# Kernel tuning notes

Hardware: AMD Instinct MI355X
Metric: run time of the kernel (lower is better)

The kernel has to match this reference:

```python
import jax, jax.numpy as jnp
import numpy as np

D_MODEL = 1024
N_HEADS = 16
HEAD_DIM = D_MODEL // N_HEADS
NEG_INF = -1e10


def setup_inputs() -> dict:
    key = jax.random.key(0)
    ks = jax.random.split(key, 6)
    B, S = 2, 2048
    x = jax.random.normal(ks[0], (B, S, D_MODEL), dtype=jnp.float32)
    mask = jnp.ones((B, S), dtype=jnp.int32)
    scale_w = 1.0 / np.sqrt(D_MODEL)
    Wq = jax.random.normal(ks[1], (D_MODEL, D_MODEL), dtype=jnp.float32) * scale_w
    Wk = jax.random.normal(ks[2], (D_MODEL, D_MODEL), dtype=jnp.float32) * scale_w
    Wv = jax.random.normal(ks[3], (D_MODEL, D_MODEL), dtype=jnp.float32) * scale_w
    Wo = jax.random.normal(ks[4], (D_MODEL, D_MODEL), dtype=jnp.float32) * scale_w
    bq = jnp.zeros((D_MODEL,), jnp.float32)
    bk = jnp.zeros((D_MODEL,), jnp.float32)
    bv = jnp.zeros((D_MODEL,), jnp.float32)
    bo = jnp.zeros((D_MODEL,), jnp.float32)
    return {"x": x, "mask": mask, "Wq": Wq, "bq": bq, "Wk": Wk, "bk": bk,
            "Wv": Wv, "bv": bv, "Wo": Wo, "bo": bo}


def reference(x, mask, Wq, bq, Wk, bk, Wv, bv, Wo, bo):
    B, S, _ = x.shape
    # Linear projections (torch Linear: y = x @ W.T + b)
    Q = x @ Wq.T + bq
    K = x @ Wk.T + bk
    V = x @ Wv.T + bv
    # [B, H, S, Dh]
    Q = Q.reshape(B, S, N_HEADS, HEAD_DIM).transpose(0, 2, 1, 3)
    K = K.reshape(B, S, N_HEADS, HEAD_DIM).transpose(0, 2, 1, 3)
    V = V.reshape(B, S, N_HEADS, HEAD_DIM).transpose(0, 2, 1, 3)
    scale = jnp.sqrt(jnp.float32(HEAD_DIM))
    energy = jnp.einsum('bhqd,bhkd->bhqk', Q, K) / scale  # [B,H,S,S]
    # mask: [B,S] -> broadcast over heads and query dim (keys masked)
    m = mask[:, None, None, :]  # [B,1,1,S]
    energy = jnp.where(m == 0, jnp.float32(NEG_INF), energy)
    attention = jax.nn.softmax(energy, axis=-1)
    # dropout in eval mode = identity
    out = jnp.einsum('bhqk,bhkd->bhqd', attention, V)  # [B,H,S,Dh]
    out = out.transpose(0, 2, 1, 3).reshape(B, S, D_MODEL)
    return out @ Wo.T + bo
```

## Files before the change

### kernel.cpp

```cpp
#include <hip/hip_runtime.h>
#include <hip/hip_bf16.h>

typedef __hip_bfloat16 bf16;
typedef __attribute__((ext_vector_type(8))) short s8v;
typedef __attribute__((ext_vector_type(4))) float f4v;

#define D_MODEL 1024
#define S_LEN   2048
#define BATCH   2
#define NH      16
#define HD      64
#define M_TOTAL 4096

__device__ __forceinline__ void gll16(const bf16* g, bf16* l) {
    __builtin_amdgcn_global_load_lds(
        (const __attribute__((address_space(1))) void*)g,
        (__attribute__((address_space(3))) void*)l, 16, 0, 0);
}

__global__ __launch_bounds__(256) void cvt_bf16x8(const float* __restrict__ s,
                                                  bf16* __restrict__ d, int n) {
    int i = (blockIdx.x * 256 + threadIdx.x) * 8;
    if (i < n) {
        float4 a = *(const float4*)(s + i);
        float4 b = *(const float4*)(s + i + 4);
        union { bf16 h[8]; uint4 u; } p;
        p.h[0] = __float2bfloat16(a.x); p.h[1] = __float2bfloat16(a.y);
        p.h[2] = __float2bfloat16(a.z); p.h[3] = __float2bfloat16(a.w);
        p.h[4] = __float2bfloat16(b.x); p.h[5] = __float2bfloat16(b.y);
        p.h[6] = __float2bfloat16(b.z); p.h[7] = __float2bfloat16(b.w);
        *(uint4*)(d + i) = p.u;
    }
}

struct WPtrs { const float* s0; const float* s1; const float* s2; const float* s3;
               bf16* d0; bf16* d1; bf16* d2; bf16* d3; };

__global__ __launch_bounds__(256) void cvt_w(WPtrs p) {
    const float* s; bf16* d;
    switch (blockIdx.y) {
        case 0:  s = p.s0; d = p.d0; break;
        case 1:  s = p.s1; d = p.d1; break;
        case 2:  s = p.s2; d = p.d2; break;
        default: s = p.s3; d = p.d3; break;
    }
    int i = (blockIdx.x * 256 + threadIdx.x) * 8;
    float4 a = *(const float4*)(s + i);
    float4 b = *(const float4*)(s + i + 4);
    union { bf16 h[8]; uint4 u; } q;
    q.h[0] = __float2bfloat16(a.x); q.h[1] = __float2bfloat16(a.y);
    q.h[2] = __float2bfloat16(a.z); q.h[3] = __float2bfloat16(a.w);
    q.h[4] = __float2bfloat16(b.x); q.h[5] = __float2bfloat16(b.y);
    q.h[6] = __float2bfloat16(b.z); q.h[7] = __float2bfloat16(b.w);
    *(uint4*)(d + i) = q.u;
}

template<int TM, int TN>
__device__ __forceinline__ void gemm_main(const bf16* __restrict__ A,
                                          const bf16* __restrict__ W,
                                          bf16* As, bf16* Bs,
                                          int bm, int bn,
                                          f4v (&acc)[TM/32][TN/32])
{
    constexpr int FM = TM / 32, FN = TN / 32;
    constexpr int CALLS_A = TM / 16, CALLS = (TM + TN) / 16, PW = CALLS / 4;
    const int t = threadIdx.x, wv = t >> 6, lane = t & 63;
    const int quad = lane >> 4, l15 = lane & 15;
    const int wm = (wv >> 1) * (TM / 2), wn = (wv & 1) * (TN / 2);
    const int lr = lane >> 2, lc = (lane & 3) * 8;

    const bf16* aptr[FM];
    const bf16* bptr[FN];
    #pragma unroll
    for (int i = 0; i < FM; ++i) aptr[i] = As + (wm + i * 16 + l15) * 32 + quad * 8;
    #pragma unroll
    for (int j = 0; j < FN; ++j) bptr[j] = Bs + (wn + j * 16 + l15) * 32 + quad * 8;

    for (int k0 = 0; k0 < D_MODEL; k0 += 32) {
        __syncthreads();
        #pragma unroll
        for (int c = 0; c < PW; ++c) {
            const int cc = wv * PW + c;
            if (cc < CALLS_A) {
                gll16(A + (size_t)(bm + cc * 16 + lr) * D_MODEL + k0 + lc,
                      As + cc * 16 * 32);
            } else {
                const int r2 = cc - CALLS_A;
                gll16(W + (size_t)(bn + r2 * 16 + lr) * D_MODEL + k0 + lc,
                      Bs + r2 * 16 * 32);
            }
        }
        __syncthreads();

        s8v af[FM], bfv[FN];
        #pragma unroll
        for (int i = 0; i < FM; ++i) af[i] = *(const s8v*)aptr[i];
        #pragma unroll
        for (int j = 0; j < FN; ++j) bfv[j] = *(const s8v*)bptr[j];
        #pragma unroll
        for (int i = 0; i < FM; ++i)
            #pragma unroll
            for (int j = 0; j < FN; ++j)
                acc[i][j] = __builtin_amdgcn_mfma_f32_16x16x32_bf16(af[i], bfv[j], acc[i][j], 0, 0, 0);
    }
}

__global__ __launch_bounds__(256) void gemm_qkv(
    const bf16* __restrict__ x,
    const bf16* __restrict__ Wq, const bf16* __restrict__ Wk, const bf16* __restrict__ Wv,
    const float* __restrict__ bq, const float* __restrict__ bk, const float* __restrict__ bv,
    bf16* __restrict__ Qb, bf16* __restrict__ Kb, bf16* __restrict__ Vtb)
{
    __shared__ __align__(16) bf16 As[128 * 32];
    __shared__ __align__(16) bf16 Bs[128 * 32];
    const int z = blockIdx.z;
    const bf16*  W    = (z == 0) ? Wq : (z == 1) ? Wk : Wv;
    const float* bias = (z == 0) ? bq : (z == 1) ? bk : bv;
    bf16*        out  = (z == 0) ? Qb : (z == 1) ? Kb : Vtb;
    const int bm = blockIdx.y * 128, bn = blockIdx.x * 128;

    f4v acc[4][4] = {};
    gemm_main<128, 128>(x, W, As, Bs, bm, bn, acc);

    const int t = threadIdx.x, wv = t >> 6, lane = t & 63;
    const int quad = lane >> 4, l15 = lane & 15;
    const int wm = (wv >> 1) * 64, wn = (wv & 1) * 64;
    #pragma unroll
    for (int j = 0; j < 4; ++j) {
        const int col = bn + wn + j * 16 + l15;
        const float bv_ = bias[col];
        const int h = col >> 6, d = col & 63;
        #pragma unroll
        for (int i = 0; i < 4; ++i) {
            #pragma unroll
            for (int r = 0; r < 4; ++r) {
                const int row = bm + wm + i * 16 + quad * 4 + r;
                const int b = row >> 11, s = row & 2047;
                const float v = acc[i][j][r] + bv_;
                size_t idx;
                if (z == 2) idx = (((size_t)(b * NH + h)) * HD + d) * S_LEN + s;
                else        idx = (((size_t)(b * NH + h)) * S_LEN + s) * HD + d;
                out[idx] = __float2bfloat16(v);
            }
        }
    }
}

__global__ __launch_bounds__(256) void gemm_out(
    const bf16* __restrict__ Ob, const bf16* __restrict__ Wo,
    const float* __restrict__ bo, float* __restrict__ out)
{
    __shared__ __align__(16) bf16 As[64 * 32];
    __shared__ __align__(16) bf16 Bs[128 * 32];
    const int bm = blockIdx.y * 64, bn = blockIdx.x * 128;

    f4v acc[2][4] = {};
    gemm_main<64, 128>(Ob, Wo, As, Bs, bm, bn, acc);

    const int t = threadIdx.x, wv = t >> 6, lane = t & 63;
    const int quad = lane >> 4, l15 = lane & 15;
    const int wm = (wv >> 1) * 32, wn = (wv & 1) * 64;
    #pragma unroll
    for (int j = 0; j < 4; ++j) {
        const int col = bn + wn + j * 16 + l15;
        const float bv_ = bo[col];
        #pragma unroll
        for (int i = 0; i < 2; ++i)
            #pragma unroll
            for (int r = 0; r < 4; ++r) {
                const int row = bm + wm + i * 16 + quad * 4 + r;
                out[(size_t)row * D_MODEL + col] = acc[i][j][r] + bv_;
            }
    }
}

__global__ __launch_bounds__(256) void attn_mfma(
    const bf16* __restrict__ Q, const bf16* __restrict__ K,
    const bf16* __restrict__ Vt, const int* __restrict__ mask,
    bf16* __restrict__ O)
{
    __shared__ __align__(16) bf16 Ks[64][72];
    __shared__ __align__(16) bf16 Vts[64][72];
    __shared__ __align__(16) bf16 Ps[4][16][72];
    __shared__ __align__(16) int  msk[64];

    const int t = threadIdx.x, wv = t >> 6, lane = t & 63;
    const int quad = lane >> 4, l15 = lane & 15;
    const int qt = blockIdx.x & 31, h = (blockIdx.x >> 5) & 15, b = blockIdx.x >> 9;
    const int q0 = qt * 64;
    const size_t qkbase = ((size_t)(b * NH + h)) * S_LEN * HD;
    const size_t vtbase = ((size_t)(b * NH + h)) * HD * S_LEN;

    const bf16* qrow = Q + qkbase + (size_t)(q0 + wv * 16 + l15) * HD;
    const s8v qf0 = *(const s8v*)(qrow + quad * 8);
    const s8v qf1 = *(const s8v*)(qrow + 32 + quad * 8);

    const int srow = t >> 2, scoff = (t & 3) * 16;

    float mprev = -1e30f, lsum = 0.f;
    f4v oacc[4] = {};

    for (int kt = 0; kt < S_LEN / 64; ++kt) {
        const int k0 = kt * 64;
        __syncthreads();
        {
            const uint4* kp = (const uint4*)(K  + qkbase + (size_t)(k0 + srow) * HD + scoff);
            const uint4* vp = (const uint4*)(Vt + vtbase + (size_t)srow * S_LEN + k0 + scoff);
            uint4 ka = kp[0], kb2 = kp[1];
            uint4 va = vp[0], vb2 = vp[1];
            *(uint4*)&Ks[srow][scoff]      = ka;
            *(uint4*)&Ks[srow][scoff + 8]  = kb2;
            *(uint4*)&Vts[srow][scoff]     = va;
            *(uint4*)&Vts[srow][scoff + 8] = vb2;
            if (t < 64) msk[t] = mask[b * S_LEN + k0 + t];
        }
        __syncthreads();

        f4v st[4];
        #pragma unroll
        for (int c = 0; c < 4; ++c) {
            s8v kf0 = *(const s8v*)&Ks[c * 16 + l15][quad * 8];
            s8v kf1 = *(const s8v*)&Ks[c * 16 + l15][32 + quad * 8];
            f4v z = {0.f, 0.f, 0.f, 0.f};
            z = __builtin_amdgcn_mfma_f32_16x16x32_bf16(kf0, qf0, z, 0, 0, 0);
            z = __builtin_amdgcn_mfma_f32_16x16x32_bf16(kf1, qf1, z, 0, 0, 0);
            st[c] = z;
        }

        float mt = -1e30f;
        #pragma unroll
        for (int c = 0; c < 4; ++c) {
            const int4 mk = *(const int4*)&msk[c * 16 + quad * 4];
            float v0 = st[c][0] * 0.125f; if (mk.x == 0) v0 = -1e10f;
            float v1 = st[c][1] * 0.125f; if (mk.y == 0) v1 = -1e10f;
            float v2 = st[c][2] * 0.125f; if (mk.z == 0) v2 = -1e10f;
            float v3 = st[c][3] * 0.125f; if (mk.w == 0) v3 = -1e10f;
            st[c][0] = v0; st[c][1] = v1; st[c][2] = v2; st[c][3] = v3;
            mt = fmaxf(mt, fmaxf(fmaxf(v0, v1), fmaxf(v2, v3)));
        }
        mt = fmaxf(mt, __shfl_xor(mt, 16, 64));
        mt = fmaxf(mt, __shfl_xor(mt, 32, 64));

        const float mn = fmaxf(mprev, mt);
        const float alpha = __expf(mprev - mn);
        mprev = mn;

        float ps = 0.f;
        #pragma unroll
        for (int c = 0; c < 4; ++c) {
            #pragma unroll
            for (int r = 0; r < 4; ++r) {
                const float p = __expf(st[c][r] - mn);
                st[c][r] = p;
                ps += p;
            }
        }
        ps += __shfl_xor(ps, 16, 64);
        ps += __shfl_xor(ps, 32, 64);
        lsum = lsum * alpha + ps;

        #pragma unroll
        for (int c = 0; c < 4; ++c) {
            union { bf16 h[4]; short4 s4; } pk;
            pk.h[0] = __float2bfloat16(st[c][0]);
            pk.h[1] = __float2bfloat16(st[c][1]);
            pk.h[2] = __float2bfloat16(st[c][2]);
            pk.h[3] = __float2bfloat16(st[c][3]);
            *(short4*)&Ps[wv][l15][c * 16 + quad * 4] = pk.s4;
        }

        float av[4];
        #pragma unroll
        for (int r = 0; r < 4; ++r) av[r] = __shfl(alpha, quad * 4 + r, 64);
        #pragma unroll
        for (int dt = 0; dt < 4; ++dt)
            #pragma unroll
            for (int r = 0; r < 4; ++r) oacc[dt][r] *= av[r];

        s8v pf0 = *(const s8v*)&Ps[wv][l15][quad * 8];
        s8v pf1 = *(const s8v*)&Ps[wv][l15][32 + quad * 8];
        #pragma unroll
        for (int dt = 0; dt < 4; ++dt) {
            s8v vf0 = *(const s8v*)&Vts[dt * 16 + l15][quad * 8];
            s8v vf1 = *(const s8v*)&Vts[dt * 16 + l15][32 + quad * 8];
            oacc[dt] = __builtin_amdgcn_mfma_f32_16x16x32_bf16(pf0, vf0, oacc[dt], 0, 0, 0);
            oacc[dt] = __builtin_amdgcn_mfma_f32_16x16x32_bf16(pf1, vf1, oacc[dt], 0, 0, 0);
        }
    }

    float linv[4];
    #pragma unroll
    for (int r = 0; r < 4; ++r) linv[r] = 1.f / __shfl(lsum, quad * 4 + r, 64);
    #pragma unroll
    for (int dt = 0; dt < 4; ++dt) {
        #pragma unroll
        for (int r = 0; r < 4; ++r) {
            const int s = q0 + wv * 16 + quad * 4 + r;
            const int col = h * 64 + dt * 16 + l15;
            O[((size_t)b * S_LEN + s) * D_MODEL + col] = __float2bfloat16(oacc[dt][r] * linv[r]);
        }
    }
}

extern "C" void kernel_launch(void* const* d_in, const int* in_sizes, int n_in,
                              void* d_out, int out_size, void* d_ws, size_t ws_size,
                              hipStream_t stream) {
    const float* x    = (const float*)d_in[0];
    const int*   mask = (const int*)  d_in[1];
    const float* Wq   = (const float*)d_in[2];
    const float* bq   = (const float*)d_in[3];
    const float* Wk   = (const float*)d_in[4];
    const float* bk   = (const float*)d_in[5];
    const float* Wv   = (const float*)d_in[6];
    const float* bv   = (const float*)d_in[7];
    const float* Wo   = (const float*)d_in[8];
    const float* bo   = (const float*)d_in[9];
    float* out = (float*)d_out;

    char* w = (char*)d_ws;
    bf16* xb  = (bf16*)w; w += (size_t)M_TOTAL * D_MODEL * 2;
    bf16* Wqb = (bf16*)w; w += (size_t)D_MODEL * D_MODEL * 2;
    bf16* Wkb = (bf16*)w; w += (size_t)D_MODEL * D_MODEL * 2;
    bf16* Wvb = (bf16*)w; w += (size_t)D_MODEL * D_MODEL * 2;
    bf16* Wob = (bf16*)w; w += (size_t)D_MODEL * D_MODEL * 2;
    bf16* Qb  = (bf16*)w; w += (size_t)M_TOTAL * D_MODEL * 2;
    bf16* Kb  = (bf16*)w; w += (size_t)M_TOTAL * D_MODEL * 2;
    bf16* Vtb = (bf16*)w; w += (size_t)M_TOTAL * D_MODEL * 2;
    bf16* Ob  = (bf16*)w; w += (size_t)M_TOTAL * D_MODEL * 2;

    const int nx = M_TOTAL * D_MODEL;
    cvt_bf16x8<<<nx / 2048, 256, 0, stream>>>(x, xb, nx);
    WPtrs wp = { Wq, Wk, Wv, Wo, Wqb, Wkb, Wvb, Wob };
    cvt_w<<<dim3(D_MODEL * D_MODEL / 2048, 4), 256, 0, stream>>>(wp);

    gemm_qkv<<<dim3(8, 32, 3), 256, 0, stream>>>(xb, Wqb, Wkb, Wvb, bq, bk, bv, Qb, Kb, Vtb);

    attn_mfma<<<BATCH * NH * (S_LEN / 64), 256, 0, stream>>>(Qb, Kb, Vtb, mask, Ob);

    gemm_out<<<dim3(8, 64), 256, 0, stream>>>(Ob, Wob, bo, out);
}
```

Measured before the change: 240.7 us.

## Use direct-to-LDS loads in attention, swap MFMA operands, fold softmax scale into Q

The attention kernel now stages K and V^T tiles with global_load_lds in a 32-wide packed layout instead of loading through registers into padded shared arrays. The PV MFMA operands are swapped so each lane holds a whole query row, which removes the alpha and lsum shuffles and lets output stores be packed short4 writes. The QKV GEMM swaps operands for Q and K so its epilogue can write packed, vectorised bf16 values, and it folds the 1/sqrt(d) scale into Q. The unpadded LDS layout may add bank conflicts on the fragment reads.

```diff
diff --git a/kernel.cpp b/kernel.cpp
--- a/kernel.cpp
+++ b/kernel.cpp
@@ -12,11 +12,9 @@
 #define HD      64
 #define M_TOTAL 4096
 
-__device__ __forceinline__ void gll16(const bf16* g, bf16* l) {
-    __builtin_amdgcn_global_load_lds(
-        (const __attribute__((address_space(1))) void*)g,
-        (__attribute__((address_space(3))) void*)l, 16, 0, 0);
-}
+#define GLL(gp, lp) __builtin_amdgcn_global_load_lds(                           \
+    (const __attribute__((address_space(1))) void*)(gp),                        \
+    (__attribute__((address_space(3))) void*)(lp), 16, 0, 0)
 
 __global__ __launch_bounds__(256) void cvt_bf16x8(const float* __restrict__ s,
                                                   bf16* __restrict__ d, int n) {
@@ -55,8 +53,8 @@
     *(uint4*)(d + i) = q.u;
 }
 
-template<int TM, int TN>
-__device__ __forceinline__ void gemm_main(const bf16* __restrict__ A,
+template<int TM, int TN, bool SWAP>
+__device__ __forceinline__ void gemm_loop(const bf16* __restrict__ A,
                                           const bf16* __restrict__ W,
                                           bf16* As, bf16* Bs,
                                           int bm, int bn,
@@ -76,18 +74,19 @@
     #pragma unroll
     for (int j = 0; j < FN; ++j) bptr[j] = Bs + (wn + j * 16 + l15) * 32 + quad * 8;
 
+    const bf16* ag = A + (size_t)(bm + lr) * D_MODEL + lc;
+    const bf16* wg = W + (size_t)(bn + lr) * D_MODEL + lc;
+
     for (int k0 = 0; k0 < D_MODEL; k0 += 32) {
         __syncthreads();
         #pragma unroll
         for (int c = 0; c < PW; ++c) {
             const int cc = wv * PW + c;
             if (cc < CALLS_A) {
-                gll16(A + (size_t)(bm + cc * 16 + lr) * D_MODEL + k0 + lc,
-                      As + cc * 16 * 32);
+                GLL(ag + (size_t)cc * 16 * D_MODEL + k0, As + cc * 512);
             } else {
                 const int r2 = cc - CALLS_A;
-                gll16(W + (size_t)(bn + r2 * 16 + lr) * D_MODEL + k0 + lc,
-                      Bs + r2 * 16 * 32);
+                GLL(wg + (size_t)r2 * 16 * D_MODEL + k0, Bs + r2 * 512);
             }
         }
         __syncthreads();
@@ -100,8 +99,12 @@
         #pragma unroll
         for (int i = 0; i < FM; ++i)
             #pragma unroll
-            for (int j = 0; j < FN; ++j)
-                acc[i][j] = __builtin_amdgcn_mfma_f32_16x16x32_bf16(af[i], bfv[j], acc[i][j], 0, 0, 0);
+            for (int j = 0; j < FN; ++j) {
+                if (SWAP)
+                    acc[i][j] = __builtin_amdgcn_mfma_f32_16x16x32_bf16(bfv[j], af[i], acc[i][j], 0, 0, 0);
+                else
+                    acc[i][j] = __builtin_amdgcn_mfma_f32_16x16x32_bf16(af[i], bfv[j], acc[i][j], 0, 0, 0);
+            }
     }
 }
 
@@ -116,31 +119,49 @@
     const int z = blockIdx.z;
     const bf16*  W    = (z == 0) ? Wq : (z == 1) ? Wk : Wv;
     const float* bias = (z == 0) ? bq : (z == 1) ? bk : bv;
-    bf16*        out  = (z == 0) ? Qb : (z == 1) ? Kb : Vtb;
     const int bm = blockIdx.y * 128, bn = blockIdx.x * 128;
-
-    f4v acc[4][4] = {};
-    gemm_main<128, 128>(x, W, As, Bs, bm, bn, acc);
 
     const int t = threadIdx.x, wv = t >> 6, lane = t & 63;
     const int quad = lane >> 4, l15 = lane & 15;
     const int wm = (wv >> 1) * 64, wn = (wv & 1) * 64;
-    #pragma unroll
-    for (int j = 0; j < 4; ++j) {
-        const int col = bn + wn + j * 16 + l15;
-        const float bv_ = bias[col];
-        const int h = col >> 6, d = col & 63;
+
+    f4v acc[4][4] = {};
+    if (z == 2) {
+        gemm_loop<128, 128, false>(x, W, As, Bs, bm, bn, acc);
+        #pragma unroll
+        for (int j = 0; j < 4; ++j) {
+            const int n = bn + wn + j * 16 + l15;
+            const int h = n >> 6, d = n & 63;
+            const float bv_ = bias[n];
+            #pragma unroll
+            for (int i = 0; i < 4; ++i) {
+                const int m0 = bm + wm + i * 16 + quad * 4;
+                const int b = m0 >> 11, s0 = m0 & 2047;
+                union { bf16 hh[4]; short4 s4; } pk;
+                #pragma unroll
+                for (int r = 0; r < 4; ++r) pk.hh[r] = __float2bfloat16(acc[i][j][r] + bv_);
+                *(short4*)&Vtb[(((size_t)(b * NH + h)) * HD + d) * S_LEN + s0] = pk.s4;
+            }
+        }
+    } else {
+        gemm_loop<128, 128, true>(x, W, As, Bs, bm, bn, acc);
+        bf16* out = (z == 0) ? Qb : Kb;
+        const float scale = (z == 0) ? 0.125f : 1.0f;
         #pragma unroll
         for (int i = 0; i < 4; ++i) {
-            #pragma unroll
-            for (int r = 0; r < 4; ++r) {
-                const int row = bm + wm + i * 16 + quad * 4 + r;
-                const int b = row >> 11, s = row & 2047;
-                const float v = acc[i][j][r] + bv_;
-                size_t idx;
-                if (z == 2) idx = (((size_t)(b * NH + h)) * HD + d) * S_LEN + s;
-                else        idx = (((size_t)(b * NH + h)) * S_LEN + s) * HD + d;
-                out[idx] = __float2bfloat16(v);
+            const int m = bm + wm + i * 16 + l15;
+            const int b = m >> 11, s = m & 2047;
+            #pragma unroll
+            for (int j = 0; j < 4; ++j) {
+                const int n0 = bn + wn + j * 16 + quad * 4;
+                const int h = n0 >> 6, d0 = n0 & 63;
+                const float4 b4 = *(const float4*)(bias + n0);
+                union { bf16 hh[4]; short4 s4; } pk;
+                pk.hh[0] = __float2bfloat16((acc[i][j][0] + b4.x) * scale);
+                pk.hh[1] = __float2bfloat16((acc[i][j][1] + b4.y) * scale);
+                pk.hh[2] = __float2bfloat16((acc[i][j][2] + b4.z) * scale);
+                pk.hh[3] = __float2bfloat16((acc[i][j][3] + b4.w) * scale);
+                *(short4*)&out[(((size_t)(b * NH + h)) * S_LEN + s) * HD + d0] = pk.s4;
             }
         }
     }
@@ -155,7 +176,7 @@
     const int bm = blockIdx.y * 64, bn = blockIdx.x * 128;
 
     f4v acc[2][4] = {};
-    gemm_main<64, 128>(Ob, Wo, As, Bs, bm, bn, acc);
+    gemm_loop<64, 128, false>(Ob, Wo, As, Bs, bm, bn, acc);
 
     const int t = threadIdx.x, wv = t >> 6, lane = t & 63;
     const int quad = lane >> 4, l15 = lane & 15;
@@ -179,9 +200,9 @@
     const bf16* __restrict__ Vt, const int* __restrict__ mask,
     bf16* __restrict__ O)
 {
-    __shared__ __align__(16) bf16 Ks[64][72];
-    __shared__ __align__(16) bf16 Vts[64][72];
-    __shared__ __align__(16) bf16 Ps[4][16][72];
+    __shared__ __align__(16) bf16 KsF[2 * 64 * 32];
+    __shared__ __align__(16) bf16 VsF[2 * 64 * 32];
+    __shared__ __align__(16) bf16 PsF[4][2 * 16 * 32];
     __shared__ __align__(16) int  msk[64];
 
     const int t = threadIdx.x, wv = t >> 6, lane = t & 63;
@@ -195,32 +216,36 @@
     const s8v qf0 = *(const s8v*)(qrow + quad * 8);
     const s8v qf1 = *(const s8v*)(qrow + 32 + quad * 8);
 
-    const int srow = t >> 2, scoff = (t & 3) * 16;
+    const int lr4 = lane >> 2, lc8 = (lane & 3) * 8;
+    const bool isK = (wv < 2);
+    const bf16* G = isK
+        ? (K  + qkbase + (size_t)lr4 * HD    + lc8 + ((wv == 1) ? 32 : 0))
+        : (Vt + vtbase + (size_t)lr4 * S_LEN + lc8 + ((wv == 3) ? 32 : 0));
+    bf16* Lb = (wv == 0) ? KsF : (wv == 1) ? (KsF + 2048)
+             : (wv == 2) ? VsF : (VsF + 2048);
+    const size_t gstride = isK ? (size_t)16 * HD : (size_t)16 * S_LEN;
+    const size_t gadv    = isK ? (size_t)64 * HD : (size_t)64;
+    const int* mrow = mask + b * S_LEN + (t & 63);
 
     float mprev = -1e30f, lsum = 0.f;
     f4v oacc[4] = {};
 
     for (int kt = 0; kt < S_LEN / 64; ++kt) {
-        const int k0 = kt * 64;
         __syncthreads();
-        {
-            const uint4* kp = (const uint4*)(K  + qkbase + (size_t)(k0 + srow) * HD + scoff);
-            const uint4* vp = (const uint4*)(Vt + vtbase + (size_t)srow * S_LEN + k0 + scoff);
-            uint4 ka = kp[0], kb2 = kp[1];
-            uint4 va = vp[0], vb2 = vp[1];
-            *(uint4*)&Ks[srow][scoff]      = ka;
-            *(uint4*)&Ks[srow][scoff + 8]  = kb2;
-            *(uint4*)&Vts[srow][scoff]     = va;
-            *(uint4*)&Vts[srow][scoff + 8] = vb2;
-            if (t < 64) msk[t] = mask[b * S_LEN + k0 + t];
-        }
+        GLL(G,               Lb);
+        GLL(G + gstride,     Lb + 512);
+        GLL(G + 2 * gstride, Lb + 1024);
+        GLL(G + 3 * gstride, Lb + 1536);
+        if (t < 64) msk[t] = mrow[kt * 64];
         __syncthreads();
 
+        G += gadv;
+
         f4v st[4];
         #pragma unroll
         for (int c = 0; c < 4; ++c) {
-            s8v kf0 = *(const s8v*)&Ks[c * 16 + l15][quad * 8];
-            s8v kf1 = *(const s8v*)&Ks[c * 16 + l15][32 + quad * 8];
+            s8v kf0 = *(const s8v*)&KsF[(c * 16 + l15) * 32 + quad * 8];
+            s8v kf1 = *(const s8v*)&KsF[2048 + (c * 16 + l15) * 32 + quad * 8];
             f4v z = {0.f, 0.f, 0.f, 0.f};
             z = __builtin_amdgcn_mfma_f32_16x16x32_bf16(kf0, qf0, z, 0, 0, 0);
             z = __builtin_amdgcn_mfma_f32_16x16x32_bf16(kf1, qf1, z, 0, 0, 0);
@@ -231,10 +256,10 @@
         #pragma unroll
         for (int c = 0; c < 4; ++c) {
             const int4 mk = *(const int4*)&msk[c * 16 + quad * 4];
-            float v0 = st[c][0] * 0.125f; if (mk.x == 0) v0 = -1e10f;
-            float v1 = st[c][1] * 0.125f; if (mk.y == 0) v1 = -1e10f;
-            float v2 = st[c][2] * 0.125f; if (mk.z == 0) v2 = -1e10f;
-            float v3 = st[c][3] * 0.125f; if (mk.w == 0) v3 = -1e10f;
+            float v0 = st[c][0]; if (mk.x == 0) v0 = -1e10f;
+            float v1 = st[c][1]; if (mk.y == 0) v1 = -1e10f;
+            float v2 = st[c][2]; if (mk.z == 0) v2 = -1e10f;
+            float v3 = st[c][3]; if (mk.w == 0) v3 = -1e10f;
             st[c][0] = v0; st[c][1] = v1; st[c][2] = v2; st[c][3] = v3;
             mt = fmaxf(mt, fmaxf(fmaxf(v0, v1), fmaxf(v2, v3)));
         }
@@ -261,44 +286,39 @@
 
         #pragma unroll
         for (int c = 0; c < 4; ++c) {
-            union { bf16 h[4]; short4 s4; } pk;
-            pk.h[0] = __float2bfloat16(st[c][0]);
-            pk.h[1] = __float2bfloat16(st[c][1]);
-            pk.h[2] = __float2bfloat16(st[c][2]);
-            pk.h[3] = __float2bfloat16(st[c][3]);
-            *(short4*)&Ps[wv][l15][c * 16 + quad * 4] = pk.s4;
-        }
-
-        float av[4];
-        #pragma unroll
-        for (int r = 0; r < 4; ++r) av[r] = __shfl(alpha, quad * 4 + r, 64);
+            union { bf16 hh[4]; short4 s4; } pk;
+            pk.hh[0] = __float2bfloat16(st[c][0]);
+            pk.hh[1] = __float2bfloat16(st[c][1]);
+            pk.hh[2] = __float2bfloat16(st[c][2]);
+            pk.hh[3] = __float2bfloat16(st[c][3]);
+            *(short4*)&PsF[wv][(c >> 1) * 512 + l15 * 32 + (c & 1) * 16 + quad * 4] = pk.s4;
+        }
+
         #pragma unroll
         for (int dt = 0; dt < 4; ++dt)
             #pragma unroll
-            for (int r = 0; r < 4; ++r) oacc[dt][r] *= av[r];
-
-        s8v pf0 = *(const s8v*)&Ps[wv][l15][quad * 8];
-        s8v pf1 = *(const s8v*)&Ps[wv][l15][32 + quad * 8];
+            for (int r = 0; r < 4; ++r) oacc[dt][r] *= alpha;
+
+        s8v pf0 = *(const s8v*)&PsF[wv][l15 * 32 + quad * 8];
+        s8v pf1 = *(const s8v*)&PsF[wv][512 + l15 * 32 + quad * 8];
         #pragma unroll
         for (int dt = 0; dt < 4; ++dt) {
-            s8v vf0 = *(const s8v*)&Vts[dt * 16 + l15][quad * 8];
-            s8v vf1 = *(const s8v*)&Vts[dt * 16 + l15][32 + quad * 8];
-            oacc[dt] = __builtin_amdgcn_mfma_f32_16x16x32_bf16(pf0, vf0, oacc[dt], 0, 0, 0);
-            oacc[dt] = __builtin_amdgcn_mfma_f32_16x16x32_bf16(pf1, vf1, oacc[dt], 0, 0, 0);
-        }
-    }
-
-    float linv[4];
-    #pragma unroll
-    for (int r = 0; r < 4; ++r) linv[r] = 1.f / __shfl(lsum, quad * 4 + r, 64);
+            s8v vf0 = *(const s8v*)&VsF[(dt * 16 + l15) * 32 + quad * 8];
+            s8v vf1 = *(const s8v*)&VsF[2048 + (dt * 16 + l15) * 32 + quad * 8];
+            oacc[dt] = __builtin_amdgcn_mfma_f32_16x16x32_bf16(vf0, pf0, oacc[dt], 0, 0, 0);
+            oacc[dt] = __builtin_amdgcn_mfma_f32_16x16x32_bf16(vf1, pf1, oacc[dt], 0, 0, 0);
+        }
+    }
+
+    const float linv = 1.f / lsum;
+    const int s = q0 + wv * 16 + l15;
+    bf16* orow = O + ((size_t)b * S_LEN + s) * D_MODEL + h * 64;
     #pragma unroll
     for (int dt = 0; dt < 4; ++dt) {
-        #pragma unroll
-        for (int r = 0; r < 4; ++r) {
-            const int s = q0 + wv * 16 + quad * 4 + r;
-            const int col = h * 64 + dt * 16 + l15;
-            O[((size_t)b * S_LEN + s) * D_MODEL + col] = __float2bfloat16(oacc[dt][r] * linv[r]);
-        }
+        union { bf16 hh[4]; short4 s4; } pk;
+        #pragma unroll
+        for (int r = 0; r < 4; ++r) pk.hh[r] = __float2bfloat16(oacc[dt][r] * linv);
+        *(short4*)&orow[dt * 16 + quad * 4] = pk.s4;
     }
 }
 
```

Result: slower. 264.1 us (+9.8%).
